# Kernel tuning notes

Hardware: AMD Instinct MI355X
Metric: run time of the kernel (lower is better)

Reference implementation:

```python
import jax, jax.numpy as jnp
import numpy as np
from jax import lax

PERM_AD = np.array([3, 0, 1, 6, 4, 2, 7, 8, 5])  # angular-difference kernel permutation
IDX_HD_POS = np.array([0, 3, 6]); IDX_HD_NEG = np.array([2, 5, 8])
IDX_VD_POS = np.array([0, 1, 2]); IDX_VD_NEG = np.array([6, 7, 8])
TOP_K = 1
THETA = 1.0


def conv2d_3x3(x, w, b):
    # x: [B,C,H,W], w: [O,I,3,3], b: [O]; stride 1, padding 1
    out = lax.conv_general_dilated(x, w, window_strides=(1, 1), padding=((1, 1), (1, 1)),
                                   dimension_numbers=('NCHW', 'OIHW', 'NCHW'))
    return out + b[None, :, None, None]


def setup_inputs() -> dict:
    key = jax.random.key(0)
    ks = jax.random.split(key, 12)
    B, C, H, W, E = 16, 64, 128, 128, 5

    def winit(k, shape, fan_in):
        return jax.random.normal(k, shape, jnp.float32) * (1.0 / np.sqrt(fan_in))

    return {
        'x': jax.random.normal(ks[0], (B, C, H, W), jnp.float32),
        'noise': jax.random.normal(ks[1], (B, E), jnp.float32),
        'w_gate': winit(ks[2], (C, E), C), 'b_gate': jnp.zeros((E,), jnp.float32),
        'w_noise': winit(ks[3], (C, E), C), 'b_noise': jnp.zeros((E,), jnp.float32),
        'w1': winit(ks[4], (C, C, 3, 3), C * 9), 'b1': jnp.zeros((C,), jnp.float32),
        'w_cd': winit(ks[5], (C, C, 3, 3), C * 9), 'b_cd': jnp.zeros((C,), jnp.float32),
        'w_hd': winit(ks[6], (C, C, 3), C * 3), 'b_hd': jnp.zeros((C,), jnp.float32),
        'w_vd': winit(ks[7], (C, C, 3), C * 3), 'b_vd': jnp.zeros((C,), jnp.float32),
        'w_ad': winit(ks[8], (C, C, 3, 3), C * 9), 'b_ad': jnp.zeros((C,), jnp.float32),
    }


def reference(x, noise, w_gate, b_gate, w_noise, b_noise,
              w1, b1, w_cd, b_cd, w_hd, b_hd, w_vd, b_vd, w_ad, b_ad):
    B, C, H, W = x.shape
    E = w_gate.shape[1]

    # ---- NoisyTopkRouter on globally pooled features ----
    pooled = x.mean(axis=(2, 3))                      # [B, C]
    logits = pooled @ w_gate + b_gate                 # [B, E]
    noise_logits = pooled @ w_noise + b_noise         # [B, E]
    noisy = logits + noise * jax.nn.softplus(noise_logits)
    topv, topi = lax.top_k(noisy, TOP_K)              # [B, k]
    sparse = jnp.full_like(noisy, -jnp.inf)
    sparse = sparse.at[jnp.arange(B)[:, None], topi].set(topv)
    gates = jax.nn.softmax(sparse, axis=-1)           # [B, E]; 0 for unselected, gate weight otherwise

    # ---- Difference-convolution expert kernels ----
    wcd_f = w_cd.reshape(C, C, 9)
    wcd = wcd_f.at[:, :, 4].add(-wcd_f.sum(-1)).reshape(C, C, 3, 3)   # center = w4 - sum(all)
    whd = jnp.zeros((C, C, 9), x.dtype).at[:, :, IDX_HD_POS].set(w_hd).at[:, :, IDX_HD_NEG].set(-w_hd).reshape(C, C, 3, 3)
    wvd = jnp.zeros((C, C, 9), x.dtype).at[:, :, IDX_VD_POS].set(w_vd).at[:, :, IDX_VD_NEG].set(-w_vd).reshape(C, C, 3, 3)
    wad_f = w_ad.reshape(C, C, 9)
    wad = (wad_f - THETA * wad_f[:, :, PERM_AD]).reshape(C, C, 3, 3)

    outs = jnp.stack([
        conv2d_3x3(x, w1, b1),
        conv2d_3x3(x, wcd, b_cd),
        conv2d_3x3(x, whd, b_hd),
        conv2d_3x3(x, wvd, b_vd),
        conv2d_3x3(x, wad, b_ad),
    ], axis=0)                                        # [E, B, C, H, W]

    # ---- SparseDispatcher.combine: per-example softmax over flattened depth, gate-weighted scatter-add ----
    flat = outs.reshape(E, B, C * H * W)
    sm = jax.nn.softmax(flat, axis=-1)                # softmax over depth dim, as in combine()
    combined = jnp.einsum('ebd,be->bd', sm, gates)    # gates are 0 for non-dispatched (expert,example) pairs
    return combined.reshape(B, C, H, W)
```

## Files before the change

kernel.cpp:

```cpp
#include <hip/hip_runtime.h>
#include <math.h>

#define B_  16
#define C_  64
#define E_  5

typedef __bf16  bf16x8 __attribute__((ext_vector_type(8)));
typedef float   f32x4  __attribute__((ext_vector_type(4)));

#define WS_WEFFB   0
#define WS_BIAS    368640
#define WS_POOL    369920
#define WS_Z       374016
#define WS_EIDX    374080
#define WS_XT      374144
#define WS_EXP     33928576ull
#define WS_NEED_A  67483008ull

static __device__ __forceinline__ unsigned short f2bf(float f) {
    unsigned int u = __float_as_uint(f);
    unsigned int r = (u + 0x7fffu + ((u >> 16) & 1u)) >> 16;
    return (unsigned short)r;
}

__global__ __launch_bounds__(256) void transpose_pool_kernel(
        const float* __restrict__ x, unsigned short* __restrict__ x_t,
        float* __restrict__ pooled) {
    int bid = blockIdx.x;
    int b = bid >> 7, row = bid & 127;
    int t = threadIdx.x;
    int wave = t >> 6, l = t & 63;
    int half = l >> 5;
    int c4 = l & 31;

    __shared__ unsigned short T[128][72];

    const float* xb = x + (size_t)b * (64 * 16384) + row * 128;

    #pragma unroll
    for (int it = 0; it < 8; it++) {
        int ci = wave * 16 + it * 2 + half;
        float4 v = *(const float4*)(xb + (size_t)ci * 16384 + c4 * 4);
        float p = v.x + v.y + v.z + v.w;
        p += __shfl_down(p, 16, 32);
        p += __shfl_down(p, 8, 32);
        p += __shfl_down(p, 4, 32);
        p += __shfl_down(p, 2, 32);
        p += __shfl_down(p, 1, 32);
        if (c4 == 0) atomicAdd(&pooled[b * 64 + ci], p * (1.0f / 16384.0f));
        int colb = c4 * 4;
        T[colb + 0][ci] = f2bf(v.x);
        T[colb + 1][ci] = f2bf(v.y);
        T[colb + 2][ci] = f2bf(v.z);
        T[colb + 3][ci] = f2bf(v.w);
    }
    __syncthreads();

    unsigned short* dst = x_t + ((size_t)(b * 128 + row) * 128) * 64;
    #pragma unroll
    for (int k = 0; k < 4; k++) {
        int chunk = t + k * 256;
        int col = chunk >> 3, c8 = chunk & 7;
        uint4 vv = *(const uint4*)&T[col][c8 * 8];
        *(uint4*)(dst + col * 64 + c8 * 8) = vv;
    }
}

__global__ __launch_bounds__(256) void prep_kernel(
        const float* __restrict__ pooled, const float* __restrict__ noise,
        const float* __restrict__ w_gate, const float* __restrict__ b_gate,
        const float* __restrict__ w_noise, const float* __restrict__ b_noise,
        const float* __restrict__ w1, const float* __restrict__ w_cd,
        const float* __restrict__ w_hd, const float* __restrict__ w_vd,
        const float* __restrict__ w_ad,
        const float* __restrict__ b1, const float* __restrict__ b_cd,
        const float* __restrict__ b_hd, const float* __restrict__ b_vd,
        const float* __restrict__ b_ad,
        int* __restrict__ expert_idx,
        unsigned short* __restrict__ wEffB, float* __restrict__ biasEff) {
    int blk = blockIdx.x;
    int t = threadIdx.x;

    if (blk < B_) {
        if (t < 64) {
            int b = blk;
            float pv = pooled[b * C_ + t];
            float ge[E_], ne[E_];
            #pragma unroll
            for (int e = 0; e < E_; e++) {
                ge[e] = pv * w_gate[t * E_ + e];
                ne[e] = pv * w_noise[t * E_ + e];
            }
            #pragma unroll
            for (int off = 32; off; off >>= 1) {
                #pragma unroll
                for (int e = 0; e < E_; e++) {
                    ge[e] += __shfl_xor(ge[e], off, 64);
                    ne[e] += __shfl_xor(ne[e], off, 64);
                }
            }
            if (t == 0) {
                float best = -1e30f; int bi = 0;
                #pragma unroll
                for (int e = 0; e < E_; e++) {
                    float lg = ge[e] + b_gate[e];
                    float nz = ne[e] + b_noise[e];
                    float sp = log1pf(expf(nz));
                    float v = lg + noise[b * E_ + e] * sp;
                    if (v > best) { best = v; bi = e; }
                }
                expert_idx[b] = bi;
            }
        }
        return;
    }

    int gid = (blk - B_) * 256 + t;
    if (gid < E_ * 36864) {
        int e   = gid / 36864;
        int r   = gid % 36864;
        int g   = r / 18432;
        int r2  = r % 18432;
        int tap = r2 / 2048;
        int r3  = r2 % 2048;
        int q   = r3 / 512;
        int r4  = r3 % 512;
        int co  = r4 / 8;
        int j   = r4 % 8;
        int ci = g * 32 + q * 8 + j;
        int base9 = (co * 64 + ci) * 9;
        int base3 = (co * 64 + ci) * 3;
        float v = 0.f;
        if (e == 0) {
            v = w1[base9 + tap];
        } else if (e == 1) {
            if (tap == 4) {
                float s = 0.f;
                #pragma unroll
                for (int k = 0; k < 9; k++) s += w_cd[base9 + k];
                v = w_cd[base9 + 4] - s;
            } else {
                v = w_cd[base9 + tap];
            }
        } else if (e == 2) {
            int m = tap % 3;
            if (m == 0) v = w_hd[base3 + tap / 3];
            else if (m == 2) v = -w_hd[base3 + tap / 3];
        } else if (e == 3) {
            if (tap < 3) v = w_vd[base3 + tap];
            else if (tap >= 6) v = -w_vd[base3 + tap - 6];
        } else {
            const int PERM[9] = {3, 0, 1, 6, 4, 2, 7, 8, 5};
            v = w_ad[base9 + tap] - w_ad[base9 + PERM[tap]];
        }
        wEffB[gid] = f2bf(v);
    } else if (gid < E_ * 36864 + E_ * 64) {
        int jj = gid - E_ * 36864;
        int e = jj / 64, co = jj % 64;
        const float* bs;
        switch (e) {
            case 0: bs = b1; break;
            case 1: bs = b_cd; break;
            case 2: bs = b_hd; break;
            case 3: bs = b_vd; break;
            default: bs = b_ad; break;
        }
        biasEff[jj] = bs[co];
    }
}

__global__ __launch_bounds__(256) void conv_mfma_kernel(
        const unsigned short* __restrict__ x_t, const unsigned short* __restrict__ wEffB,
        const float* __restrict__ biasEff, const int* __restrict__ expert_idx,
        unsigned short* __restrict__ expw, float* __restrict__ outf,
        float* __restrict__ Z, int direct_f32) {
    int bid = blockIdx.x;
    int b = bid >> 6;
    int rem = bid & 63;
    int rg = rem >> 1;
    int ch = rem & 1;

    int t = threadIdx.x;
    int wave = t >> 6;
    int lane = t & 63;
    int ln = lane & 15;
    int q = lane >> 4;

    int e = expert_idx[b];

    __shared__ __align__(16) unsigned short A_lds[9 * 4 * 66 * 8];
    __shared__ __align__(16) unsigned short Xs[6 * 4 * 68 * 8];
    __shared__ float zs[4];

    f32x4 acc[4][4];
    #pragma unroll
    for (int i = 0; i < 4; i++)
        #pragma unroll
        for (int jn = 0; jn < 4; jn++)
            acc[i][jn] = (f32x4){0.f, 0.f, 0.f, 0.f};

    const unsigned short* xb = x_t + (size_t)b * (128 * 128 * 64);
    const unsigned short* we = wEffB + (size_t)e * 36864;

    for (int g = 0; g < 2; g++) {
        const uint4* asrc = (const uint4*)(we + g * 18432);
        for (int j = t; j < 2304; j += 256) {
            int slotrow = j >> 6;
            int m = j & 63;
            *(uint4*)&A_lds[(slotrow * 66 + m) * 8] = asrc[j];
        }
        for (int j = t; j < 1584; j += 256) {
            int xr = j / 264;
            int r2 = j % 264;
            int col = r2 >> 2;
            int qq = r2 & 3;
            int irow = rg * 4 - 1 + xr;
            int icol = ch * 64 - 1 + col;
            uint4 v = make_uint4(0, 0, 0, 0);
            if ((unsigned)irow < 128u && (unsigned)icol < 128u)
                v = *(const uint4*)(xb + ((size_t)irow * 128 + icol) * 64 + g * 32 + qq * 8);
            *(uint4*)&Xs[((xr * 4 + qq) * 68 + col) * 8] = v;
        }
        __syncthreads();

        #pragma unroll
        for (int tap = 0; tap < 9; tap++) {
            int dr = tap / 3, dc = tap % 3;
            bf16x8 af[4], bfr[4];
            #pragma unroll
            for (int mt = 0; mt < 4; mt++)
                af[mt] = *(const bf16x8*)&A_lds[((tap * 4 + q) * 66 + mt * 16 + ln) * 8];
            int xr = wave + dr;
            #pragma unroll
            for (int t4 = 0; t4 < 4; t4++)
                bfr[t4] = *(const bf16x8*)&Xs[((xr * 4 + q) * 68 + t4 * 16 + ln + dc) * 8];
            #pragma unroll
            for (int mt = 0; mt < 4; mt++)
                #pragma unroll
                for (int t4 = 0; t4 < 4; t4++)
                    acc[mt][t4] = __builtin_amdgcn_mfma_f32_16x16x32_bf16(
                        af[mt], bfr[t4], acc[mt][t4], 0, 0, 0);
        }
        __syncthreads();
    }

    int orow = rg * 4 + wave;
    float bsum = 0.f;
    size_t obase = (size_t)b * (64 * 16384);
    #pragma unroll
    for (int mt = 0; mt < 4; mt++) {
        float4 bias4 = *(const float4*)(biasEff + e * 64 + mt * 16 + q * 4);
        const float* bp = (const float*)&bias4;
        #pragma unroll
        for (int r = 0; r < 4; r++) {
            int co = mt * 16 + q * 4 + r;
            size_t cb = obase + (size_t)co * 16384 + (size_t)orow * 128;
            #pragma unroll
            for (int t4 = 0; t4 < 4; t4++) {
                float ev = __expf(acc[mt][t4][r] + bp[r]);
                bsum += ev;
                int ocol = ch * 64 + t4 * 16 + ln;
                if (direct_f32) outf[cb + ocol] = ev;
                else            expw[cb + ocol] = f2bf(ev);
            }
        }
    }
    for (int off = 32; off; off >>= 1) bsum += __shfl_down(bsum, off, 64);
    if (lane == 0) zs[wave] = bsum;
    __syncthreads();
    if (t == 0) atomicAdd(&Z[b], zs[0] + zs[1] + zs[2] + zs[3]);
}

#define N_UINT4 2097152
__global__ __launch_bounds__(256) void scale_bf16_kernel(
        const unsigned short* __restrict__ expw, const float* __restrict__ Z,
        float* __restrict__ out) {
    __shared__ float sinv[B_];
    if (threadIdx.x < B_) sinv[threadIdx.x] = 1.0f / Z[threadIdx.x];
    __syncthreads();
    for (int gid = blockIdx.x * 256 + threadIdx.x; gid < N_UINT4; gid += 2048 * 256) {
        int b = gid >> 17;
        float s = sinv[b];
        uint4 r = ((const uint4*)expw)[gid];
        float4 o0, o1;
        o0.x = __uint_as_float(r.x << 16) * s;
        o0.y = __uint_as_float(r.x & 0xffff0000u) * s;
        o0.z = __uint_as_float(r.y << 16) * s;
        o0.w = __uint_as_float(r.y & 0xffff0000u) * s;
        o1.x = __uint_as_float(r.z << 16) * s;
        o1.y = __uint_as_float(r.z & 0xffff0000u) * s;
        o1.z = __uint_as_float(r.w << 16) * s;
        o1.w = __uint_as_float(r.w & 0xffff0000u) * s;
        ((float4*)out)[gid * 2] = o0;
        ((float4*)out)[gid * 2 + 1] = o1;
    }
}

#define N_FLOAT4 4194304
__global__ __launch_bounds__(256) void scale_inplace_kernel(
        float* __restrict__ out, const float* __restrict__ Z) {
    __shared__ float sinv[B_];
    if (threadIdx.x < B_) sinv[threadIdx.x] = 1.0f / Z[threadIdx.x];
    __syncthreads();
    for (int gid = blockIdx.x * 256 + threadIdx.x; gid < N_FLOAT4; gid += 2048 * 256) {
        int b = gid >> 18;
        float s = sinv[b];
        float4 v = ((float4*)out)[gid];
        v.x *= s; v.y *= s; v.z *= s; v.w *= s;
        ((float4*)out)[gid] = v;
    }
}

extern "C" void kernel_launch(void* const* d_in, const int* in_sizes, int n_in,
                              void* d_out, int out_size, void* d_ws, size_t ws_size,
                              hipStream_t stream) {
    const float* x       = (const float*)d_in[0];
    const float* noise   = (const float*)d_in[1];
    const float* w_gate  = (const float*)d_in[2];
    const float* b_gate  = (const float*)d_in[3];
    const float* w_noise = (const float*)d_in[4];
    const float* b_noise = (const float*)d_in[5];
    const float* w1      = (const float*)d_in[6];
    const float* b1      = (const float*)d_in[7];
    const float* w_cd    = (const float*)d_in[8];
    const float* b_cd    = (const float*)d_in[9];
    const float* w_hd    = (const float*)d_in[10];
    const float* b_hd    = (const float*)d_in[11];
    const float* w_vd    = (const float*)d_in[12];
    const float* b_vd    = (const float*)d_in[13];
    const float* w_ad    = (const float*)d_in[14];
    const float* b_ad    = (const float*)d_in[15];

    char* ws = (char*)d_ws;
    unsigned short* wEffB   = (unsigned short*)(ws + WS_WEFFB);
    float*          biasEff = (float*)(ws + WS_BIAS);
    float*          pooled  = (float*)(ws + WS_POOL);
    float*          Zbuf    = (float*)(ws + WS_Z);
    int*            eidx    = (int*)(ws + WS_EIDX);
    unsigned short* x_t     = (unsigned short*)(ws + WS_XT);
    unsigned short* expw    = (unsigned short*)(ws + WS_EXP);

    float* out = (float*)d_out;
    int mode_a = (ws_size >= WS_NEED_A) ? 1 : 0;

    hipMemsetAsync(pooled, 0, 4160, stream);

    transpose_pool_kernel<<<B_ * 128, 256, 0, stream>>>(x, x_t, pooled);
    prep_kernel<<<B_ + 722, 256, 0, stream>>>(pooled, noise, w_gate, b_gate,
                                              w_noise, b_noise,
                                              w1, w_cd, w_hd, w_vd, w_ad,
                                              b1, b_cd, b_hd, b_vd, b_ad,
                                              eidx, wEffB, biasEff);
    conv_mfma_kernel<<<1024, 256, 0, stream>>>(x_t, wEffB, biasEff, eidx,
                                               expw, out, Zbuf, mode_a ? 0 : 1);
    if (mode_a)
        scale_bf16_kernel<<<2048, 256, 0, stream>>>(expw, Zbuf, out);
    else
        scale_inplace_kernel<<<2048, 256, 0, stream>>>(out, Zbuf);
}
```

Measured before the change: 220.1 us.

## Fuse weight prep into transpose, route in conv, read X directly from global

Merges the effective-weight and bias build into the transpose/pool kernel as extra blocks, and moves the top-1 router computation into the conv kernel, so the separate prep kernel launch goes away. The conv kernel stops staging the input tile in LDS and instead loads each tap's B fragments straight from global/L2. It also adds an occupancy hint of 4 blocks per SM. This removes one launch and an LDS staging pass, but every block now recomputes the router, and the input is re-fetched from cache nine times per tap set rather than reused from shared memory.

```diff
diff --git a/kernel.cpp b/kernel.cpp
--- a/kernel.cpp
+++ b/kernel.cpp
@@ -12,10 +12,10 @@
 #define WS_BIAS    368640
 #define WS_POOL    369920
 #define WS_Z       374016
-#define WS_EIDX    374080
-#define WS_XT      374144
-#define WS_EXP     33928576ull
-#define WS_NEED_A  67483008ull
+#define WS_CNT     374080
+#define WS_XT      376128
+#define WS_EXP     33930560ull
+#define WS_NEED_A  67484992ull
 
 static __device__ __forceinline__ unsigned short f2bf(float f) {
     unsigned int u = __float_as_uint(f);
@@ -23,12 +23,76 @@
     return (unsigned short)r;
 }
 
-__global__ __launch_bounds__(256) void transpose_pool_kernel(
+__global__ __launch_bounds__(256) void transpose_build_kernel(
         const float* __restrict__ x, unsigned short* __restrict__ x_t,
-        float* __restrict__ pooled) {
+        float* __restrict__ pooled,
+        const float* __restrict__ w1, const float* __restrict__ w_cd,
+        const float* __restrict__ w_hd, const float* __restrict__ w_vd,
+        const float* __restrict__ w_ad,
+        const float* __restrict__ b1, const float* __restrict__ b_cd,
+        const float* __restrict__ b_hd, const float* __restrict__ b_vd,
+        const float* __restrict__ b_ad,
+        unsigned short* __restrict__ wEffB, float* __restrict__ biasEff) {
     int bid = blockIdx.x;
+    int t = threadIdx.x;
+
+    if (bid >= 2048) {
+        int gid = (bid - 2048) * 256 + t;
+        if (gid < E_ * 36864) {
+            int e   = gid / 36864;
+            int r   = gid % 36864;
+            int g   = r / 18432;
+            int r2  = r % 18432;
+            int tap = r2 / 2048;
+            int r3  = r2 % 2048;
+            int q   = r3 / 512;
+            int r4  = r3 % 512;
+            int co  = r4 / 8;
+            int j   = r4 % 8;
+            int ci = g * 32 + q * 8 + j;
+            int base9 = (co * 64 + ci) * 9;
+            int base3 = (co * 64 + ci) * 3;
+            float v = 0.f;
+            if (e == 0) {
+                v = w1[base9 + tap];
+            } else if (e == 1) {
+                if (tap == 4) {
+                    float s = 0.f;
+                    #pragma unroll
+                    for (int k = 0; k < 9; k++) s += w_cd[base9 + k];
+                    v = w_cd[base9 + 4] - s;
+                } else {
+                    v = w_cd[base9 + tap];
+                }
+            } else if (e == 2) {
+                int m = tap % 3;
+                if (m == 0) v = w_hd[base3 + tap / 3];
+                else if (m == 2) v = -w_hd[base3 + tap / 3];
+            } else if (e == 3) {
+                if (tap < 3) v = w_vd[base3 + tap];
+                else if (tap >= 6) v = -w_vd[base3 + tap - 6];
+            } else {
+                const int PERM[9] = {3, 0, 1, 6, 4, 2, 7, 8, 5};
+                v = w_ad[base9 + tap] - w_ad[base9 + PERM[tap]];
+            }
+            wEffB[gid] = f2bf(v);
+        } else if (gid < E_ * 36864 + E_ * 64) {
+            int jj = gid - E_ * 36864;
+            int e = jj / 64, co = jj % 64;
+            const float* bs;
+            switch (e) {
+                case 0: bs = b1; break;
+                case 1: bs = b_cd; break;
+                case 2: bs = b_hd; break;
+                case 3: bs = b_vd; break;
+                default: bs = b_ad; break;
+            }
+            biasEff[jj] = bs[co];
+        }
+        return;
+    }
+
     int b = bid >> 7, row = bid & 127;
-    int t = threadIdx.x;
     int wave = t >> 6, l = t & 63;
     int half = l >> 5;
     int c4 = l & 31;
@@ -66,112 +130,12 @@
     }
 }
 
-__global__ __launch_bounds__(256) void prep_kernel(
+__global__ __launch_bounds__(256, 4) void conv_mfma_kernel(
+        const unsigned short* __restrict__ x_t, const unsigned short* __restrict__ wEffB,
+        const float* __restrict__ biasEff,
         const float* __restrict__ pooled, const float* __restrict__ noise,
         const float* __restrict__ w_gate, const float* __restrict__ b_gate,
         const float* __restrict__ w_noise, const float* __restrict__ b_noise,
-        const float* __restrict__ w1, const float* __restrict__ w_cd,
-        const float* __restrict__ w_hd, const float* __restrict__ w_vd,
-        const float* __restrict__ w_ad,
-        const float* __restrict__ b1, const float* __restrict__ b_cd,
-        const float* __restrict__ b_hd, const float* __restrict__ b_vd,
-        const float* __restrict__ b_ad,
-        int* __restrict__ expert_idx,
-        unsigned short* __restrict__ wEffB, float* __restrict__ biasEff) {
-    int blk = blockIdx.x;
-    int t = threadIdx.x;
-
-    if (blk < B_) {
-        if (t < 64) {
-            int b = blk;
-            float pv = pooled[b * C_ + t];
-            float ge[E_], ne[E_];
-            #pragma unroll
-            for (int e = 0; e < E_; e++) {
-                ge[e] = pv * w_gate[t * E_ + e];
-                ne[e] = pv * w_noise[t * E_ + e];
-            }
-            #pragma unroll
-            for (int off = 32; off; off >>= 1) {
-                #pragma unroll
-                for (int e = 0; e < E_; e++) {
-                    ge[e] += __shfl_xor(ge[e], off, 64);
-                    ne[e] += __shfl_xor(ne[e], off, 64);
-                }
-            }
-            if (t == 0) {
-                float best = -1e30f; int bi = 0;
-                #pragma unroll
-                for (int e = 0; e < E_; e++) {
-                    float lg = ge[e] + b_gate[e];
-                    float nz = ne[e] + b_noise[e];
-                    float sp = log1pf(expf(nz));
-                    float v = lg + noise[b * E_ + e] * sp;
-                    if (v > best) { best = v; bi = e; }
-                }
-                expert_idx[b] = bi;
-            }
-        }
-        return;
-    }
-
-    int gid = (blk - B_) * 256 + t;
-    if (gid < E_ * 36864) {
-        int e   = gid / 36864;
-        int r   = gid % 36864;
-        int g   = r / 18432;
-        int r2  = r % 18432;
-        int tap = r2 / 2048;
-        int r3  = r2 % 2048;
-        int q   = r3 / 512;
-        int r4  = r3 % 512;
-        int co  = r4 / 8;
-        int j   = r4 % 8;
-        int ci = g * 32 + q * 8 + j;
-        int base9 = (co * 64 + ci) * 9;
-        int base3 = (co * 64 + ci) * 3;
-        float v = 0.f;
-        if (e == 0) {
-            v = w1[base9 + tap];
-        } else if (e == 1) {
-            if (tap == 4) {
-                float s = 0.f;
-                #pragma unroll
-                for (int k = 0; k < 9; k++) s += w_cd[base9 + k];
-                v = w_cd[base9 + 4] - s;
-            } else {
-                v = w_cd[base9 + tap];
-            }
-        } else if (e == 2) {
-            int m = tap % 3;
-            if (m == 0) v = w_hd[base3 + tap / 3];
-            else if (m == 2) v = -w_hd[base3 + tap / 3];
-        } else if (e == 3) {
-            if (tap < 3) v = w_vd[base3 + tap];
-            else if (tap >= 6) v = -w_vd[base3 + tap - 6];
-        } else {
-            const int PERM[9] = {3, 0, 1, 6, 4, 2, 7, 8, 5};
-            v = w_ad[base9 + tap] - w_ad[base9 + PERM[tap]];
-        }
-        wEffB[gid] = f2bf(v);
-    } else if (gid < E_ * 36864 + E_ * 64) {
-        int jj = gid - E_ * 36864;
-        int e = jj / 64, co = jj % 64;
-        const float* bs;
-        switch (e) {
-            case 0: bs = b1; break;
-            case 1: bs = b_cd; break;
-            case 2: bs = b_hd; break;
-            case 3: bs = b_vd; break;
-            default: bs = b_ad; break;
-        }
-        biasEff[jj] = bs[co];
-    }
-}
-
-__global__ __launch_bounds__(256) void conv_mfma_kernel(
-        const unsigned short* __restrict__ x_t, const unsigned short* __restrict__ wEffB,
-        const float* __restrict__ biasEff, const int* __restrict__ expert_idx,
         unsigned short* __restrict__ expw, float* __restrict__ outf,
         float* __restrict__ Z, int direct_f32) {
     int bid = blockIdx.x;
@@ -186,11 +150,41 @@
     int ln = lane & 15;
     int q = lane >> 4;
 
-    int e = expert_idx[b];
-
     __shared__ __align__(16) unsigned short A_lds[9 * 4 * 66 * 8];
-    __shared__ __align__(16) unsigned short Xs[6 * 4 * 68 * 8];
     __shared__ float zs[4];
+    __shared__ int   se_sh;
+
+    if (wave == 0) {
+        float pv = pooled[b * C_ + lane];
+        float ge[E_], ne[E_];
+        #pragma unroll
+        for (int e = 0; e < E_; e++) {
+            ge[e] = pv * w_gate[lane * E_ + e];
+            ne[e] = pv * w_noise[lane * E_ + e];
+        }
+        #pragma unroll
+        for (int off = 32; off; off >>= 1) {
+            #pragma unroll
+            for (int e = 0; e < E_; e++) {
+                ge[e] += __shfl_xor(ge[e], off, 64);
+                ne[e] += __shfl_xor(ne[e], off, 64);
+            }
+        }
+        if (lane == 0) {
+            float best = -1e30f; int bi = 0;
+            #pragma unroll
+            for (int e = 0; e < E_; e++) {
+                float lg = ge[e] + b_gate[e];
+                float nz = ne[e] + b_noise[e];
+                float sp = log1pf(expf(nz));
+                float v = lg + noise[b * E_ + e] * sp;
+                if (v > best) { best = v; bi = e; }
+            }
+            se_sh = bi;
+        }
+    }
+    __syncthreads();
+    int e = se_sh;
 
     f32x4 acc[4][4];
     #pragma unroll
@@ -203,37 +197,36 @@
     const unsigned short* we = wEffB + (size_t)e * 36864;
 
     for (int g = 0; g < 2; g++) {
+        if (g) __syncthreads();
         const uint4* asrc = (const uint4*)(we + g * 18432);
         for (int j = t; j < 2304; j += 256) {
             int slotrow = j >> 6;
             int m = j & 63;
             *(uint4*)&A_lds[(slotrow * 66 + m) * 8] = asrc[j];
         }
-        for (int j = t; j < 1584; j += 256) {
-            int xr = j / 264;
-            int r2 = j % 264;
-            int col = r2 >> 2;
-            int qq = r2 & 3;
-            int irow = rg * 4 - 1 + xr;
-            int icol = ch * 64 - 1 + col;
-            uint4 v = make_uint4(0, 0, 0, 0);
-            if ((unsigned)irow < 128u && (unsigned)icol < 128u)
-                v = *(const uint4*)(xb + ((size_t)irow * 128 + icol) * 64 + g * 32 + qq * 8);
-            *(uint4*)&Xs[((xr * 4 + qq) * 68 + col) * 8] = v;
-        }
         __syncthreads();
 
         #pragma unroll
         for (int tap = 0; tap < 9; tap++) {
             int dr = tap / 3, dc = tap % 3;
+            int irow = rg * 4 - 1 + wave + dr;
+            bool rok = (unsigned)irow < 128u;
+            const unsigned short* xrow = xb + (long long)irow * (128 * 64) + g * 32 + q * 8;
+            int icol0 = ch * 64 - 1 + ln + dc;
+
             bf16x8 af[4], bfr[4];
+            #pragma unroll
+            for (int t4 = 0; t4 < 4; t4++) {
+                int icol = icol0 + t4 * 16;
+                uint4 raw = make_uint4(0, 0, 0, 0);
+                if (rok && (unsigned)icol < 128u)
+                    raw = *(const uint4*)(xrow + (size_t)icol * 64);
+                bfr[t4] = *(bf16x8*)&raw;
+            }
             #pragma unroll
             for (int mt = 0; mt < 4; mt++)
                 af[mt] = *(const bf16x8*)&A_lds[((tap * 4 + q) * 66 + mt * 16 + ln) * 8];
-            int xr = wave + dr;
-            #pragma unroll
-            for (int t4 = 0; t4 < 4; t4++)
-                bfr[t4] = *(const bf16x8*)&Xs[((xr * 4 + q) * 68 + t4 * 16 + ln + dc) * 8];
+
             #pragma unroll
             for (int mt = 0; mt < 4; mt++)
                 #pragma unroll
@@ -241,7 +234,6 @@
                     acc[mt][t4] = __builtin_amdgcn_mfma_f32_16x16x32_bf16(
                         af[mt], bfr[t4], acc[mt][t4], 0, 0, 0);
         }
-        __syncthreads();
     }
 
     int orow = rg * 4 + wave;
@@ -336,7 +328,6 @@
     float*          biasEff = (float*)(ws + WS_BIAS);
     float*          pooled  = (float*)(ws + WS_POOL);
     float*          Zbuf    = (float*)(ws + WS_Z);
-    int*            eidx    = (int*)(ws + WS_EIDX);
     unsigned short* x_t     = (unsigned short*)(ws + WS_XT);
     unsigned short* expw    = (unsigned short*)(ws + WS_EXP);
 
@@ -345,14 +336,14 @@
 
     hipMemsetAsync(pooled, 0, 4160, stream);
 
-    transpose_pool_kernel<<<B_ * 128, 256, 0, stream>>>(x, x_t, pooled);
-    prep_kernel<<<B_ + 722, 256, 0, stream>>>(pooled, noise, w_gate, b_gate,
-                                              w_noise, b_noise,
-                                              w1, w_cd, w_hd, w_vd, w_ad,
-                                              b1, b_cd, b_hd, b_vd, b_ad,
-                                              eidx, wEffB, biasEff);
-    conv_mfma_kernel<<<1024, 256, 0, stream>>>(x_t, wEffB, biasEff, eidx,
-                                               expw, out, Zbuf, mode_a ? 0 : 1);
+    transpose_build_kernel<<<2048 + 722, 256, 0, stream>>>(
+        x, x_t, pooled, w1, w_cd, w_hd, w_vd, w_ad,
+        b1, b_cd, b_hd, b_vd, b_ad, wEffB, biasEff);
+
+    conv_mfma_kernel<<<1024, 256, 0, stream>>>(
+        x_t, wEffB, biasEff, pooled, noise, w_gate, b_gate, w_noise, b_noise,
+        expw, out, Zbuf, mode_a ? 0 : 1);
+
     if (mode_a)
         scale_bf16_kernel<<<2048, 256, 0, stream>>>(expw, Zbuf, out);
     else
```

Result: slower. 272.0 us (+23.6%).
